# Kernel tuning notes

Measured on AMD Instinct MI355X. Metric: run time of the kernel, lower is better.

The kernel has to match this reference:

```python
import jax, jax.numpy as jnp
import numpy as np

NUM_USERS = 100000
NUM_ITEMS = 50000
NUM_EDGES = 1000000
EMB_DIM = 64


def setup_inputs() -> dict:
    key = jax.random.key(0)
    k1, k2, k3, k4, k5, k6 = jax.random.split(key, 6)
    return {
        "user_emb": jax.random.normal(k1, (NUM_USERS, EMB_DIM), dtype=jnp.float32),
        "item_emb": jax.random.normal(k2, (NUM_ITEMS, EMB_DIM), dtype=jnp.float32),
        "u_sw": jax.random.uniform(k3, (NUM_USERS, 1), dtype=jnp.float32),
        "i_sw": jax.random.uniform(k4, (NUM_ITEMS, 1), dtype=jnp.float32),
        "edge_src_user": jax.random.randint(k5, (NUM_EDGES,), 0, NUM_USERS, dtype=jnp.int32),
        "edge_dst_item": jax.random.randint(k6, (NUM_EDGES,), 0, NUM_ITEMS, dtype=jnp.int32),
    }


def _segment_mean(feat_src, src_idx, dst_idx, num_dst, inv_deg):
    # gather source node features onto edges, sum-reduce at destinations, divide by degree
    s = jax.ops.segment_sum(feat_src[src_idx], dst_idx, num_segments=num_dst)
    return s * inv_deg


def reference(user_emb, item_emb, u_sw, i_sw, edge_src_user, edge_dst_item):
    ones = jnp.ones((edge_src_user.shape[0],), dtype=user_emb.dtype)
    deg_i = jax.ops.segment_sum(ones, edge_dst_item, num_segments=NUM_ITEMS)
    deg_u = jax.ops.segment_sum(ones, edge_src_user, num_segments=NUM_USERS)
    # DGL mean gives 0 for zero-degree nodes
    inv_deg_i = jnp.where(deg_i > 0, 1.0 / jnp.maximum(deg_i, 1.0), 0.0)[:, None]
    inv_deg_u = jnp.where(deg_u > 0, 1.0 / jnp.maximum(deg_u, 1.0), 0.0)[:, None]

    def one_round(u, i):
        # 'like': user -> item mean aggregation; 'rev_like': item -> user
        new_i = _segment_mean(u, edge_src_user, edge_dst_item, NUM_ITEMS, inv_deg_i)
        new_u = _segment_mean(i, edge_dst_item, edge_src_user, NUM_USERS, inv_deg_u)
        return new_u + u * u_sw, new_i + i * i_sw

    u, i = one_round(user_emb, item_emb)
    u, i = one_round(u, i)
    return (u, i)
```

## Files before the change

### kernel.cpp

```cpp
#include <hip/hip_runtime.h>

#define NU 100000
#define NI 50000
#define NE 1000000
#define D  64
#define NBI 196
#define NBU 391
#define NB_TOT (NBI + NBU)
#define CHUNK 4096

__device__ __forceinline__ unsigned short f2bf(float f) {
    unsigned int u = __float_as_uint(f);
    u += 0x7FFFu + ((u >> 16) & 1u);
    return (unsigned short)(u >> 16);
}
__device__ __forceinline__ float bf2f(unsigned short h) {
    return __uint_as_float(((unsigned int)h) << 16);
}

__global__ void k_bhist(const int* __restrict__ esrc, const int* __restrict__ edst,
                        int* __restrict__ bcnt, int ne) {
    __shared__ int h[NB_TOT];
    for (int b = threadIdx.x; b < NB_TOT; b += blockDim.x) h[b] = 0;
    __syncthreads();
    int stride = gridDim.x * blockDim.x;
    for (int e = blockIdx.x * blockDim.x + threadIdx.x; e < ne; e += stride) {
        atomicAdd(&h[edst[e] >> 8], 1);
        atomicAdd(&h[NBI + (esrc[e] >> 8)], 1);
    }
    __syncthreads();
    for (int b = threadIdx.x; b < NB_TOT; b += blockDim.x) {
        int v = h[b];
        if (v) atomicAdd(&bcnt[b], v);
    }
}

__global__ void k_bscan_both(const int* __restrict__ bcnt,
                             int* __restrict__ bbase_i, int* __restrict__ gcur_i,
                             int* __restrict__ bbase_u, int* __restrict__ gcur_u) {
    __shared__ int s[512];
    int tid = threadIdx.x;
    const int* in = (blockIdx.x == 0) ? bcnt : bcnt + NBI;
    int nb        = (blockIdx.x == 0) ? NBI : NBU;
    int* bbase    = (blockIdx.x == 0) ? bbase_i : bbase_u;
    int* gcur     = (blockIdx.x == 0) ? gcur_i : gcur_u;
    int v = (tid < nb) ? in[tid] : 0;
    s[tid] = v;
    __syncthreads();
    for (int o = 1; o < 512; o <<= 1) {
        int t = (tid >= o) ? s[tid - o] : 0;
        __syncthreads();
        s[tid] += t;
        __syncthreads();
    }
    if (tid < nb) { int ex = s[tid] - v; bbase[tid] = ex; gcur[tid] = ex; }
    if (tid == 0) bbase[nb] = NE;
}

__global__ void k_part_both(const int* __restrict__ esrc, const int* __restrict__ edst,
                            int* __restrict__ gcur_i, int* __restrict__ gcur_u,
                            unsigned int* __restrict__ rec_i, unsigned int* __restrict__ rec_u) {
    __shared__ int cnt_i[NBI], gb_i[NBI], cnt_u[NBU], gb_u[NBU];
    int tid = threadIdx.x;
    for (int b = tid; b < NBI; b += 256) cnt_i[b] = 0;
    for (int b = tid; b < NBU; b += 256) cnt_u[b] = 0;
    __syncthreads();
    int base = blockIdx.x * CHUNK;
    int dd[16], uu[16], ki[16], ku[16];
#pragma unroll
    for (int k = 0; k < 16; k++) {
        int j = base + tid + k * 256;
        dd[k] = -1;
        if (j < NE) {
            dd[k] = edst[j]; uu[k] = esrc[j];
            ki[k] = atomicAdd(&cnt_i[dd[k] >> 8], 1);
            ku[k] = atomicAdd(&cnt_u[uu[k] >> 8], 1);
        }
    }
    __syncthreads();
    for (int b = tid; b < NBI; b += 256) { int v = cnt_i[b]; if (v) gb_i[b] = atomicAdd(&gcur_i[b], v); }
    for (int b = tid; b < NBU; b += 256) { int v = cnt_u[b]; if (v) gb_u[b] = atomicAdd(&gcur_u[b], v); }
    __syncthreads();
#pragma unroll
    for (int k = 0; k < 16; k++) {
        if (dd[k] >= 0) {
            rec_i[gb_i[dd[k] >> 8] + ki[k]] = ((unsigned int)(dd[k] & 255) << 17) | (unsigned int)uu[k];
            rec_u[gb_u[uu[k] >> 8] + ku[k]] = ((unsigned int)(uu[k] & 255) << 17) | (unsigned int)dd[k];
        }
    }
}

__global__ void k_local_both(const unsigned int* __restrict__ rec_i, const unsigned int* __restrict__ rec_u,
                             const int* __restrict__ bbase_i, const int* __restrict__ bbase_u,
                             int* __restrict__ rp_i, int* __restrict__ rp_u,
                             int* __restrict__ col_i, int* __restrict__ col_u) {
    __shared__ int cnt[256];
    __shared__ int off[256];
    int tid = threadIdx.x;
    int t = blockIdx.x;
    bool item = t < NBI;
    int b = item ? t : t - NBI;
    const unsigned int* rec = item ? rec_i : rec_u;
    const int* bb = item ? bbase_i : bbase_u;
    int* rp  = item ? rp_i : rp_u;
    int* col = item ? col_i : col_u;
    int nn   = item ? NI : NU;
    int beg = bb[b], end = bb[b + 1];
    cnt[tid] = 0;
    __syncthreads();
    for (int j = beg + tid; j < end; j += 256)
        atomicAdd(&cnt[rec[j] >> 17], 1);
    __syncthreads();
    int v = cnt[tid];
    off[tid] = v;
    __syncthreads();
    for (int o = 1; o < 256; o <<= 1) {
        int tv = (tid >= o) ? off[tid - o] : 0;
        __syncthreads();
        off[tid] += tv;
        __syncthreads();
    }
    int ex = off[tid] - v;
    int node = b * 256 + tid;
    if (node <= nn) rp[node] = beg + ex;
    cnt[tid] = ex;
    __syncthreads();
    for (int j = beg + tid; j < end; j += 256) {
        unsigned int r = rec[j];
        int p = atomicAdd(&cnt[r >> 17], 1);
        col[beg + p] = (int)(r & 0x1FFFF);
    }
}

__device__ __forceinline__ void agg_g_f32(const float* __restrict__ feat,
        const float* __restrict__ self, const float* __restrict__ sw,
        const int* __restrict__ rp, const int* __restrict__ cols,
        float* __restrict__ out, unsigned short* __restrict__ out_bf,
        int n, int li, int lb) {
    int beg = rp[n], end = rp[n + 1];
    float4 a = make_float4(0.f, 0.f, 0.f, 0.f);
    for (int j0 = beg; j0 < end; j0 += 16) {
        int cv = (j0 + li < end) ? cols[j0 + li] : 0;
        int nj = end - j0; if (nj > 16) nj = 16;
        int j = 0;
        for (; j + 4 <= nj; j += 4) {
            int c0 = __shfl(cv, lb + j,     64);
            int c1 = __shfl(cv, lb + j + 1, 64);
            int c2 = __shfl(cv, lb + j + 2, 64);
            int c3 = __shfl(cv, lb + j + 3, 64);
            float4 f0 = *(const float4*)(feat + (size_t)c0 * D + li * 4);
            float4 f1 = *(const float4*)(feat + (size_t)c1 * D + li * 4);
            float4 f2 = *(const float4*)(feat + (size_t)c2 * D + li * 4);
            float4 f3 = *(const float4*)(feat + (size_t)c3 * D + li * 4);
            a.x += f0.x + f1.x + f2.x + f3.x;
            a.y += f0.y + f1.y + f2.y + f3.y;
            a.z += f0.z + f1.z + f2.z + f3.z;
            a.w += f0.w + f1.w + f2.w + f3.w;
        }
        for (; j < nj; ++j) {
            int c = __shfl(cv, lb + j, 64);
            float4 f = *(const float4*)(feat + (size_t)c * D + li * 4);
            a.x += f.x; a.y += f.y; a.z += f.z; a.w += f.w;
        }
    }
    int dgr = end - beg;
    float inv = (dgr > 0) ? (1.0f / (float)dgr) : 0.0f;
    float swv = sw[n];
    float4 s = *(const float4*)(self + (size_t)n * D + li * 4);
    float4 r;
    r.x = a.x * inv + s.x * swv;
    r.y = a.y * inv + s.y * swv;
    r.z = a.z * inv + s.z * swv;
    r.w = a.w * inv + s.w * swv;
    *(float4*)(out + (size_t)n * D + li * 4) = r;
    if (out_bf) {
        ushort4 hb;
        hb.x = f2bf(r.x); hb.y = f2bf(r.y); hb.z = f2bf(r.z); hb.w = f2bf(r.w);
        *(ushort4*)(out_bf + (size_t)n * D + li * 4) = hb;
    }
}

__device__ __forceinline__ void agg_g_bf(const unsigned short* __restrict__ feat,
        const float* __restrict__ self, const float* __restrict__ sw,
        const int* __restrict__ rp, const int* __restrict__ cols,
        float* __restrict__ out, int n, int li, int lb) {
    int beg = rp[n], end = rp[n + 1];
    float4 a = make_float4(0.f, 0.f, 0.f, 0.f);
    for (int j0 = beg; j0 < end; j0 += 16) {
        int cv = (j0 + li < end) ? cols[j0 + li] : 0;
        int nj = end - j0; if (nj > 16) nj = 16;
        int j = 0;
        for (; j + 4 <= nj; j += 4) {
            int c0 = __shfl(cv, lb + j,     64);
            int c1 = __shfl(cv, lb + j + 1, 64);
            int c2 = __shfl(cv, lb + j + 2, 64);
            int c3 = __shfl(cv, lb + j + 3, 64);
            ushort4 h0 = *(const ushort4*)(feat + (size_t)c0 * D + li * 4);
            ushort4 h1 = *(const ushort4*)(feat + (size_t)c1 * D + li * 4);
            ushort4 h2 = *(const ushort4*)(feat + (size_t)c2 * D + li * 4);
            ushort4 h3 = *(const ushort4*)(feat + (size_t)c3 * D + li * 4);
            a.x += bf2f(h0.x) + bf2f(h1.x) + bf2f(h2.x) + bf2f(h3.x);
            a.y += bf2f(h0.y) + bf2f(h1.y) + bf2f(h2.y) + bf2f(h3.y);
            a.z += bf2f(h0.z) + bf2f(h1.z) + bf2f(h2.z) + bf2f(h3.z);
            a.w += bf2f(h0.w) + bf2f(h1.w) + bf2f(h2.w) + bf2f(h3.w);
        }
        for (; j < nj; ++j) {
            int c = __shfl(cv, lb + j, 64);
            ushort4 h = *(const ushort4*)(feat + (size_t)c * D + li * 4);
            a.x += bf2f(h.x); a.y += bf2f(h.y); a.z += bf2f(h.z); a.w += bf2f(h.w);
        }
    }
    int dgr = end - beg;
    float inv = (dgr > 0) ? (1.0f / (float)dgr) : 0.0f;
    float swv = sw[n];
    float4 s = *(const float4*)(self + (size_t)n * D + li * 4);
    float4 r;
    r.x = a.x * inv + s.x * swv;
    r.y = a.y * inv + s.y * swv;
    r.z = a.z * inv + s.z * swv;
    r.w = a.w * inv + s.w * swv;
    *(float4*)(out + (size_t)n * D + li * 4) = r;
}

__global__ void k_agg_r1(const float* __restrict__ user_emb, const float* __restrict__ item_emb,
                         const float* __restrict__ u_sw, const float* __restrict__ i_sw,
                         const int* __restrict__ rp_i, const int* __restrict__ rp_u,
                         const int* __restrict__ col_i, const int* __restrict__ col_u,
                         float* out_i, float* out_u,
                         unsigned short* i1_bf, unsigned short* u1_bf) {
    int g  = (blockIdx.x * blockDim.x + threadIdx.x) >> 4;
    int li = threadIdx.x & 15;
    int lb = threadIdx.x & 48;
    if (g < NI)
        agg_g_f32(user_emb, item_emb, i_sw, rp_i, col_i, out_i, i1_bf, g, li, lb);
    else if (g < NI + NU)
        agg_g_f32(item_emb, user_emb, u_sw, rp_u, col_u, out_u, u1_bf, g - NI, li, lb);
}

__global__ void k_agg_r2(const unsigned short* __restrict__ u1_bf, const unsigned short* __restrict__ i1_bf,
                         const float* __restrict__ u_sw, const float* __restrict__ i_sw,
                         const int* __restrict__ rp_i, const int* __restrict__ rp_u,
                         const int* __restrict__ col_i, const int* __restrict__ col_u,
                         float* out_i, float* out_u) {
    int g  = (blockIdx.x * blockDim.x + threadIdx.x) >> 4;
    int li = threadIdx.x & 15;
    int lb = threadIdx.x & 48;
    if (g < NI)
        agg_g_bf(u1_bf, out_i, i_sw, rp_i, col_i, out_i, g, li, lb);
    else if (g < NI + NU)
        agg_g_bf(i1_bf, out_u, u_sw, rp_u, col_u, out_u, g - NI, li, lb);
}

extern "C" void kernel_launch(void* const* d_in, const int* in_sizes, int n_in,
                              void* d_out, int out_size, void* d_ws, size_t ws_size,
                              hipStream_t stream) {
    const float* user_emb = (const float*)d_in[0];
    const float* item_emb = (const float*)d_in[1];
    const float* u_sw     = (const float*)d_in[2];
    const float* i_sw     = (const float*)d_in[3];
    const int*   esrc     = (const int*)d_in[4];
    const int*   edst     = (const int*)d_in[5];

    float* out_u = (float*)d_out;
    float* out_i = out_u + NU * D;

    int* bcnt    = (int*)d_ws;
    int* bbase_i = bcnt + NB_TOT;
    int* bbase_u = bbase_i + NBI + 1;
    int* gcur_i  = bbase_u + NBU + 1;
    int* gcur_u  = gcur_i + NBI;
    int* rp_i    = gcur_u + NBU;
    int* rp_u    = rp_i + NI + 1;
    int* col_i   = rp_u + NU + 1;
    int* col_u   = col_i + NE;
    uintptr_t pa = ((uintptr_t)(col_u + NE) + 15) & ~(uintptr_t)15;
    unsigned short* u1_bf = (unsigned short*)pa;
    unsigned short* i1_bf = u1_bf + (size_t)NU * D;
    unsigned int* rec_i = (unsigned int*)pa;
    unsigned int* rec_u = rec_i + NE;

    hipMemsetAsync(bcnt, 0, NB_TOT * sizeof(int), stream);

    const int B = 256;

    k_bhist<<<512, B, 0, stream>>>(esrc, edst, bcnt, NE);
    k_bscan_both<<<2, 512, 0, stream>>>(bcnt, bbase_i, gcur_i, bbase_u, gcur_u);
    k_part_both<<<(NE + CHUNK - 1) / CHUNK, B, 0, stream>>>(esrc, edst, gcur_i, gcur_u, rec_i, rec_u);
    k_local_both<<<NB_TOT, B, 0, stream>>>(rec_i, rec_u, bbase_i, bbase_u, rp_i, rp_u, col_i, col_u);

    int gblocks = ((NI + NU) * 16 + B - 1) / B;

    k_agg_r1<<<gblocks, B, 0, stream>>>(user_emb, item_emb, u_sw, i_sw,
                                        rp_i, rp_u, col_i, col_u,
                                        out_i, out_u, i1_bf, u1_bf);
    k_agg_r2<<<gblocks, B, 0, stream>>>(u1_bf, i1_bf, u_sw, i_sw,
                                        rp_i, rp_u, col_i, col_u,
                                        out_i, out_u);
}
```

Before: 279.5 us.

## Convert embeddings to fp16 up front and run all gathers in half precision

Converts the input user and item embeddings to fp16 inside the histogram kernel, then gathers from fp16 in both rounds. Previously round 1 gathered fp32 and round 2 gathered bf16. Round 1 is split into separate item and user kernels so the user output can overwrite u0h in place, and round-1 fp32 outputs are no longer written. This halves round-1 gather traffic and removes one fp32 write, at the cost of an extra conversion pass and lower precision (fp16 range and rounding) on the inputs.

```diff
diff --git a/kernel.cpp b/kernel.cpp
--- a/kernel.cpp
+++ b/kernel.cpp
@@ -1,4 +1,5 @@
 #include <hip/hip_runtime.h>
+#include <hip/hip_fp16.h>
 
 #define NU 100000
 #define NI 50000
@@ -9,24 +10,39 @@
 #define NB_TOT (NBI + NBU)
 #define CHUNK 4096
 
-__device__ __forceinline__ unsigned short f2bf(float f) {
-    unsigned int u = __float_as_uint(f);
-    u += 0x7FFFu + ((u >> 16) & 1u);
-    return (unsigned short)(u >> 16);
-}
-__device__ __forceinline__ float bf2f(unsigned short h) {
-    return __uint_as_float(((unsigned int)h) << 16);
-}
-
-__global__ void k_bhist(const int* __restrict__ esrc, const int* __restrict__ edst,
-                        int* __restrict__ bcnt, int ne) {
+__device__ __forceinline__ unsigned short f2h(float f) {
+    return __half_as_ushort(__float2half(f));
+}
+__device__ __forceinline__ float h2f(unsigned short h) {
+    return __half2float(__ushort_as_half(h));
+}
+
+__global__ void k_bhist_cvt(const int* __restrict__ esrc, const int* __restrict__ edst,
+                            int* __restrict__ bcnt,
+                            const float* __restrict__ ue, const float* __restrict__ ie,
+                            unsigned short* __restrict__ u0h, unsigned short* __restrict__ i0h) {
     __shared__ int h[NB_TOT];
     for (int b = threadIdx.x; b < NB_TOT; b += blockDim.x) h[b] = 0;
     __syncthreads();
-    int stride = gridDim.x * blockDim.x;
-    for (int e = blockIdx.x * blockDim.x + threadIdx.x; e < ne; e += stride) {
+    int gt = blockIdx.x * blockDim.x + threadIdx.x;
+    int gs = gridDim.x * blockDim.x;
+    for (int e = gt; e < NE; e += gs) {
         atomicAdd(&h[edst[e] >> 8], 1);
         atomicAdd(&h[NBI + (esrc[e] >> 8)], 1);
+    }
+    const float4* uf = (const float4*)ue;
+    ushort4* uh = (ushort4*)u0h;
+    for (int i = gt; i < NU * (D / 4); i += gs) {
+        float4 v = uf[i];
+        ushort4 o; o.x = f2h(v.x); o.y = f2h(v.y); o.z = f2h(v.z); o.w = f2h(v.w);
+        uh[i] = o;
+    }
+    const float4* if4 = (const float4*)ie;
+    ushort4* ih = (ushort4*)i0h;
+    for (int i = gt; i < NI * (D / 4); i += gs) {
+        float4 v = if4[i];
+        ushort4 o; o.x = f2h(v.x); o.y = f2h(v.y); o.z = f2h(v.z); o.w = f2h(v.w);
+        ih[i] = o;
     }
     __syncthreads();
     for (int b = threadIdx.x; b < NB_TOT; b += blockDim.x) {
@@ -132,60 +148,14 @@
     }
 }
 
-__device__ __forceinline__ void agg_g_f32(const float* __restrict__ feat,
-        const float* __restrict__ self, const float* __restrict__ sw,
+template<bool WF, bool WH>
+__device__ __forceinline__ void agg_h(const unsigned short* __restrict__ feat,
+        const unsigned short* selfh, const float* __restrict__ sw,
         const int* __restrict__ rp, const int* __restrict__ cols,
-        float* __restrict__ out, unsigned short* __restrict__ out_bf,
+        float* __restrict__ outf, unsigned short* outh,
         int n, int li, int lb) {
     int beg = rp[n], end = rp[n + 1];
-    float4 a = make_float4(0.f, 0.f, 0.f, 0.f);
-    for (int j0 = beg; j0 < end; j0 += 16) {
-        int cv = (j0 + li < end) ? cols[j0 + li] : 0;
-        int nj = end - j0; if (nj > 16) nj = 16;
-        int j = 0;
-        for (; j + 4 <= nj; j += 4) {
-            int c0 = __shfl(cv, lb + j,     64);
-            int c1 = __shfl(cv, lb + j + 1, 64);
-            int c2 = __shfl(cv, lb + j + 2, 64);
-            int c3 = __shfl(cv, lb + j + 3, 64);
-            float4 f0 = *(const float4*)(feat + (size_t)c0 * D + li * 4);
-            float4 f1 = *(const float4*)(feat + (size_t)c1 * D + li * 4);
-            float4 f2 = *(const float4*)(feat + (size_t)c2 * D + li * 4);
-            float4 f3 = *(const float4*)(feat + (size_t)c3 * D + li * 4);
-            a.x += f0.x + f1.x + f2.x + f3.x;
-            a.y += f0.y + f1.y + f2.y + f3.y;
-            a.z += f0.z + f1.z + f2.z + f3.z;
-            a.w += f0.w + f1.w + f2.w + f3.w;
-        }
-        for (; j < nj; ++j) {
-            int c = __shfl(cv, lb + j, 64);
-            float4 f = *(const float4*)(feat + (size_t)c * D + li * 4);
-            a.x += f.x; a.y += f.y; a.z += f.z; a.w += f.w;
-        }
-    }
-    int dgr = end - beg;
-    float inv = (dgr > 0) ? (1.0f / (float)dgr) : 0.0f;
-    float swv = sw[n];
-    float4 s = *(const float4*)(self + (size_t)n * D + li * 4);
-    float4 r;
-    r.x = a.x * inv + s.x * swv;
-    r.y = a.y * inv + s.y * swv;
-    r.z = a.z * inv + s.z * swv;
-    r.w = a.w * inv + s.w * swv;
-    *(float4*)(out + (size_t)n * D + li * 4) = r;
-    if (out_bf) {
-        ushort4 hb;
-        hb.x = f2bf(r.x); hb.y = f2bf(r.y); hb.z = f2bf(r.z); hb.w = f2bf(r.w);
-        *(ushort4*)(out_bf + (size_t)n * D + li * 4) = hb;
-    }
-}
-
-__device__ __forceinline__ void agg_g_bf(const unsigned short* __restrict__ feat,
-        const float* __restrict__ self, const float* __restrict__ sw,
-        const int* __restrict__ rp, const int* __restrict__ cols,
-        float* __restrict__ out, int n, int li, int lb) {
-    int beg = rp[n], end = rp[n + 1];
-    float4 a = make_float4(0.f, 0.f, 0.f, 0.f);
+    float ax = 0.f, ay = 0.f, az = 0.f, aw = 0.f;
     for (int j0 = beg; j0 < end; j0 += 16) {
         int cv = (j0 + li < end) ? cols[j0 + li] : 0;
         int nj = end - j0; if (nj > 16) nj = 16;
@@ -199,56 +169,65 @@
             ushort4 h1 = *(const ushort4*)(feat + (size_t)c1 * D + li * 4);
             ushort4 h2 = *(const ushort4*)(feat + (size_t)c2 * D + li * 4);
             ushort4 h3 = *(const ushort4*)(feat + (size_t)c3 * D + li * 4);
-            a.x += bf2f(h0.x) + bf2f(h1.x) + bf2f(h2.x) + bf2f(h3.x);
-            a.y += bf2f(h0.y) + bf2f(h1.y) + bf2f(h2.y) + bf2f(h3.y);
-            a.z += bf2f(h0.z) + bf2f(h1.z) + bf2f(h2.z) + bf2f(h3.z);
-            a.w += bf2f(h0.w) + bf2f(h1.w) + bf2f(h2.w) + bf2f(h3.w);
+            ax += h2f(h0.x) + h2f(h1.x) + h2f(h2.x) + h2f(h3.x);
+            ay += h2f(h0.y) + h2f(h1.y) + h2f(h2.y) + h2f(h3.y);
+            az += h2f(h0.z) + h2f(h1.z) + h2f(h2.z) + h2f(h3.z);
+            aw += h2f(h0.w) + h2f(h1.w) + h2f(h2.w) + h2f(h3.w);
         }
         for (; j < nj; ++j) {
             int c = __shfl(cv, lb + j, 64);
             ushort4 h = *(const ushort4*)(feat + (size_t)c * D + li * 4);
-            a.x += bf2f(h.x); a.y += bf2f(h.y); a.z += bf2f(h.z); a.w += bf2f(h.w);
+            ax += h2f(h.x); ay += h2f(h.y); az += h2f(h.z); aw += h2f(h.w);
         }
     }
     int dgr = end - beg;
     float inv = (dgr > 0) ? (1.0f / (float)dgr) : 0.0f;
     float swv = sw[n];
-    float4 s = *(const float4*)(self + (size_t)n * D + li * 4);
-    float4 r;
-    r.x = a.x * inv + s.x * swv;
-    r.y = a.y * inv + s.y * swv;
-    r.z = a.z * inv + s.z * swv;
-    r.w = a.w * inv + s.w * swv;
-    *(float4*)(out + (size_t)n * D + li * 4) = r;
-}
-
-__global__ void k_agg_r1(const float* __restrict__ user_emb, const float* __restrict__ item_emb,
+    ushort4 s4 = *(const ushort4*)(selfh + (size_t)n * D + li * 4);
+    float rx = ax * inv + h2f(s4.x) * swv;
+    float ry = ay * inv + h2f(s4.y) * swv;
+    float rz = az * inv + h2f(s4.z) * swv;
+    float rw = aw * inv + h2f(s4.w) * swv;
+    if (WH) {
+        ushort4 o; o.x = f2h(rx); o.y = f2h(ry); o.z = f2h(rz); o.w = f2h(rw);
+        *(ushort4*)(outh + (size_t)n * D + li * 4) = o;
+    }
+    if (WF) {
+        float4 o; o.x = rx; o.y = ry; o.z = rz; o.w = rw;
+        *(float4*)(outf + (size_t)n * D + li * 4) = o;
+    }
+}
+
+__global__ void k_agg_r1i(const unsigned short* __restrict__ u0h, const unsigned short* __restrict__ i0h,
+                          const float* __restrict__ i_sw,
+                          const int* __restrict__ rp_i, const int* __restrict__ col_i,
+                          unsigned short* __restrict__ i1h) {
+    int g  = (blockIdx.x * blockDim.x + threadIdx.x) >> 4;
+    if (g >= NI) return;
+    agg_h<false, true>(u0h, i0h, i_sw, rp_i, col_i, nullptr, i1h, g, threadIdx.x & 15, threadIdx.x & 48);
+}
+
+__global__ void k_agg_r1u(const unsigned short* __restrict__ i0h, const unsigned short* u0h,
+                          const float* __restrict__ u_sw,
+                          const int* __restrict__ rp_u, const int* __restrict__ col_u,
+                          unsigned short* u1h) {
+    int g  = (blockIdx.x * blockDim.x + threadIdx.x) >> 4;
+    if (g >= NU) return;
+    agg_h<false, true>(i0h, u0h, u_sw, rp_u, col_u, nullptr, u1h, g, threadIdx.x & 15, threadIdx.x & 48);
+}
+
+__global__ void k_agg_r2(const unsigned short* __restrict__ u1h, const unsigned short* __restrict__ i1h,
                          const float* __restrict__ u_sw, const float* __restrict__ i_sw,
                          const int* __restrict__ rp_i, const int* __restrict__ rp_u,
                          const int* __restrict__ col_i, const int* __restrict__ col_u,
-                         float* out_i, float* out_u,
-                         unsigned short* i1_bf, unsigned short* u1_bf) {
+                         float* __restrict__ out_i, float* __restrict__ out_u) {
     int g  = (blockIdx.x * blockDim.x + threadIdx.x) >> 4;
     int li = threadIdx.x & 15;
     int lb = threadIdx.x & 48;
     if (g < NI)
-        agg_g_f32(user_emb, item_emb, i_sw, rp_i, col_i, out_i, i1_bf, g, li, lb);
+        agg_h<true, false>(u1h, i1h, i_sw, rp_i, col_i, out_i, nullptr, g, li, lb);
     else if (g < NI + NU)
-        agg_g_f32(item_emb, user_emb, u_sw, rp_u, col_u, out_u, u1_bf, g - NI, li, lb);
-}
-
-__global__ void k_agg_r2(const unsigned short* __restrict__ u1_bf, const unsigned short* __restrict__ i1_bf,
-                         const float* __restrict__ u_sw, const float* __restrict__ i_sw,
-                         const int* __restrict__ rp_i, const int* __restrict__ rp_u,
-                         const int* __restrict__ col_i, const int* __restrict__ col_u,
-                         float* out_i, float* out_u) {
-    int g  = (blockIdx.x * blockDim.x + threadIdx.x) >> 4;
-    int li = threadIdx.x & 15;
-    int lb = threadIdx.x & 48;
-    if (g < NI)
-        agg_g_bf(u1_bf, out_i, i_sw, rp_i, col_i, out_i, g, li, lb);
-    else if (g < NI + NU)
-        agg_g_bf(i1_bf, out_u, u_sw, rp_u, col_u, out_u, g - NI, li, lb);
+        agg_h<true, false>(i1h, u1h, u_sw, rp_u, col_u, out_u, nullptr, g - NI, li, lb);
 }
 
 extern "C" void kernel_launch(void* const* d_in, const int* in_sizes, int n_in,
@@ -274,26 +253,26 @@
     int* col_i   = rp_u + NU + 1;
     int* col_u   = col_i + NE;
     uintptr_t pa = ((uintptr_t)(col_u + NE) + 15) & ~(uintptr_t)15;
-    unsigned short* u1_bf = (unsigned short*)pa;
-    unsigned short* i1_bf = u1_bf + (size_t)NU * D;
-    unsigned int* rec_i = (unsigned int*)pa;
+    unsigned short* u0h = (unsigned short*)pa;
+    unsigned short* i0h = u0h + (size_t)NU * D;
+    uintptr_t pc = (uintptr_t)(i0h + (size_t)NI * D);
+    unsigned int* rec_i = (unsigned int*)pc;
     unsigned int* rec_u = rec_i + NE;
+    unsigned short* i1h = (unsigned short*)pc;
+    unsigned short* u1h = u0h;
 
     hipMemsetAsync(bcnt, 0, NB_TOT * sizeof(int), stream);
 
     const int B = 256;
 
-    k_bhist<<<512, B, 0, stream>>>(esrc, edst, bcnt, NE);
+    k_bhist_cvt<<<1024, B, 0, stream>>>(esrc, edst, bcnt, user_emb, item_emb, u0h, i0h);
     k_bscan_both<<<2, 512, 0, stream>>>(bcnt, bbase_i, gcur_i, bbase_u, gcur_u);
     k_part_both<<<(NE + CHUNK - 1) / CHUNK, B, 0, stream>>>(esrc, edst, gcur_i, gcur_u, rec_i, rec_u);
     k_local_both<<<NB_TOT, B, 0, stream>>>(rec_i, rec_u, bbase_i, bbase_u, rp_i, rp_u, col_i, col_u);
 
-    int gblocks = ((NI + NU) * 16 + B - 1) / B;
-
-    k_agg_r1<<<gblocks, B, 0, stream>>>(user_emb, item_emb, u_sw, i_sw,
-                                        rp_i, rp_u, col_i, col_u,
-                                        out_i, out_u, i1_bf, u1_bf);
-    k_agg_r2<<<gblocks, B, 0, stream>>>(u1_bf, i1_bf, u_sw, i_sw,
-                                        rp_i, rp_u, col_i, col_u,
-                                        out_i, out_u);
-}
+    k_agg_r1i<<<(NI * 16) / B, B, 0, stream>>>(u0h, i0h, i_sw, rp_i, col_i, i1h);
+    k_agg_r1u<<<(NU * 16) / B, B, 0, stream>>>(i0h, u0h, u_sw, rp_u, col_u, u1h);
+    k_agg_r2<<<((NI + NU) * 16) / B, B, 0, stream>>>(u1h, i1h, u_sw, i_sw,
+                                                     rp_i, rp_u, col_i, col_u,
+                                                     out_i, out_u);
+}
```

New measurement: 276.6 us (median of 2 runs). About the same (-1.0%).
